# Kernel optimization log

Measured on AMD Instinct MI355X. Metric: run time of the kernel, lower is better.

## Reference

```python
import jax, jax.numpy as jnp
import numpy as np

N_USER, N_ITEM, D, N_LAYER, NNZ, B = 50000, 100000, 64, 3, 2400000, 4096
NEG_SLOPE = 0.2
EPS = 1e-12


def setup_inputs() -> dict:
    key = jax.random.key(0)
    ks = jax.random.split(key, 12)
    N = N_USER + N_ITEM
    user_emb = jax.random.normal(ks[0], (N_USER, D), dtype=jnp.float32) * 0.1
    item_emb = jax.random.normal(ks[1], (N_ITEM, D), dtype=jnp.float32) * 0.1
    rows = jax.random.randint(ks[2], (NNZ,), 0, N, dtype=jnp.int32)
    cols = jax.random.randint(ks[3], (NNZ,), 0, N, dtype=jnp.int32)
    edge_index = jnp.stack([rows, cols])  # [2, nnz] COO indices of sparse L
    # normalized-Laplacian-like positive values, ~1/deg scale
    edge_vals = jax.random.uniform(ks[4], (NNZ,), dtype=jnp.float32) * (1.0 / 16.0)
    scale = 1.0 / np.sqrt(D)
    W1 = jax.random.normal(ks[5], (N_LAYER, D, D), dtype=jnp.float32) * scale
    W2 = jax.random.normal(ks[6], (N_LAYER, D, D), dtype=jnp.float32) * scale
    b1 = jnp.zeros((N_LAYER, D), dtype=jnp.float32)
    b2 = jnp.zeros((N_LAYER, D), dtype=jnp.float32)
    users = jax.random.randint(ks[7], (B,), 1, N_USER + 1, dtype=jnp.int32)      # 1-indexed
    pos_items = jax.random.randint(ks[8], (B,), 1, N_ITEM + 1, dtype=jnp.int32)  # 1-indexed
    neg_items = jax.random.randint(ks[9], (B,), 1, N_ITEM + 1, dtype=jnp.int32)  # 1-indexed
    return {"user_emb": user_emb, "item_emb": item_emb, "edge_vals": edge_vals,
            "W1": W1, "b1": b1, "W2": W2, "b2": b2,
            "edge_index": edge_index, "users": users,
            "pos_items": pos_items, "neg_items": neg_items}


def _spmm(rows, cols, vals, E, num_nodes):
    # sparse COO L @ E : gather source rows, scale by edge value, scatter-add to dest rows
    return jax.ops.segment_sum(vals[:, None] * E[cols], rows, num_segments=num_nodes)


def reference(user_emb, item_emb, edge_vals, W1, b1, W2, b2,
              edge_index, users, pos_items, neg_items):
    n_user = user_emb.shape[0]
    N = n_user + item_emb.shape[0]
    rows, cols = edge_index[0], edge_index[1]
    E = jnp.concatenate([user_emb, item_emb], axis=0)  # [N, d]
    all_E = [E]
    for i in range(W1.shape[0]):
        LE = _spmm(rows, cols, edge_vals, E, N)          # L @ E
        # (L + I) @ E @ W1 + (L@E * E) @ W2  (dropouts are eval-mode identity)
        h = (LE + E) @ W1[i] + b1[i] + (LE * E) @ W2[i] + b2[i]
        E = jax.nn.leaky_relu(h, NEG_SLOPE)
        nrm = jnp.maximum(jnp.linalg.norm(E, axis=1, keepdims=True), EPS)
        all_E.append(E / nrm)  # L2-normalized copy stored; unnormalized E propagates
    all_E = jnp.concatenate(all_E, axis=1)               # [N, d*(1+L)]
    u_emb = all_E[:n_user][users - 1]
    items = all_E[n_user:]
    return u_emb, items[pos_items - 1], items[neg_items - 1]
```

## Files before the change

kernel.cpp:

```cpp
#include <hip/hip_runtime.h>

#define N_USERC 50000
#define N_ITEMC 100000
#define NN      150000
#define DD      64
#define NLAYER  3
#define NNZC    2400000
#define BB      4096
#define NRID    (3*BB)
#define NBKT    147
#define NABLK   586
#define NTILE   4688
#define ELLW    32
#define ELLROWS 150528
#define OVCAP   32768
#define NWPB    97
#define NPREPB  (NWPB + NABLK)
#define NIB     9375
#define NOSB    3072
#define NISB    (NIB + NOSB)

typedef unsigned short ushort_t;
typedef __attribute__((ext_vector_type(8))) short bf16x8;
typedef __attribute__((ext_vector_type(4))) float f32x4;

static __device__ __forceinline__ float bf2f(ushort_t b) {
    unsigned int u = ((unsigned int)b) << 16;
    return __uint_as_float(u);
}
static __device__ __forceinline__ ushort_t f2bf(float f) {
    unsigned int u = __float_as_uint(f);
    u = u + 0x7FFFu + ((u >> 16) & 1u);
    return (ushort_t)(u >> 16);
}

__global__ __launch_bounds__(256) void k_sniffzb(const unsigned int* __restrict__ ue_words,
                                                 int* __restrict__ flag,
                                                 int* __restrict__ bucket_cnt,
                                                 int* __restrict__ ovcnt) {
    int t = threadIdx.x;
    if (t < 64) {
        int cnt = 0;
        for (int i = 0; i < 4; i++) {
            unsigned int w = ue_words[t * 4 + i];
            unsigned int lo = w & 0xFFFFu;
            unsigned int ex = (lo >> 7) & 0xFF;
            if (ex >= 100 && ex <= 132) cnt++;
        }
        for (int m = 1; m < 64; m <<= 1) cnt += __shfl_xor(cnt, m, 64);
        if (t == 0) *flag = (cnt >= 128) ? 1 : 0;
    } else if (t - 64 < NBKT) {
        bucket_cnt[t - 64] = 0;
    } else if (t == 255) {
        *ovcnt = 0;
    }
}

__global__ __launch_bounds__(256) void k_prep(const void* __restrict__ W1,
                                              const void* __restrict__ W2,
                                              const void* __restrict__ b1,
                                              const void* __restrict__ b2,
                                              const int* __restrict__ rows,
                                              const int* __restrict__ flag,
                                              ushort_t* __restrict__ Wfrag,
                                              float* __restrict__ bsum,
                                              int* __restrict__ bucket_cnt) {
    __shared__ int h[NBKT];
    if (blockIdx.x < NWPB) {
        int idx = blockIdx.x * 256 + threadIdx.x;
        int isbf = *flag;
        if (idx < NLAYER * 4 * 4 * 64 * 8) {
            int i    = idx & 7;
            int lane = (idx >> 3) & 63;
            int jt   = (idx >> 9) & 3;
            int s    = (idx >> 11) & 3;
            int l    = idx >> 13;
            int kfull = 32 * (s & 1) + 8 * (lane >> 4) + i;
            int col   = jt * 16 + (lane & 15);
            const void* W = (s < 2) ? W1 : W2;
            size_t off = (size_t)l * 4096 + (size_t)kfull * 64 + col;
            float v = isbf ? bf2f(((const ushort_t*)W)[off]) : ((const float*)W)[off];
            Wfrag[idx] = f2bf(v);
        } else {
            int r = idx - NLAYER * 4 * 4 * 64 * 8;
            if (r < NLAYER * 64) {
                float v1 = isbf ? bf2f(((const ushort_t*)b1)[r]) : ((const float*)b1)[r];
                float v2 = isbf ? bf2f(((const ushort_t*)b2)[r]) : ((const float*)b2)[r];
                bsum[r] = v1 + v2;
            }
        }
    } else {
        int t = threadIdx.x;
        if (t < NBKT) h[t] = 0;
        __syncthreads();
        int e0 = (blockIdx.x - NWPB) * 4096;
#pragma unroll
        for (int i = 0; i < 16; i++) {
            int e = e0 + t + i * 256;
            if (e < NNZC) atomicAdd(&h[rows[e] >> 10], 1);
        }
        __syncthreads();
        if (t < NBKT && h[t]) atomicAdd(&bucket_cnt[t], h[t]);
    }
}

__global__ __launch_bounds__(256) void k_bscan(const int* __restrict__ bucket_cnt,
                                               int* __restrict__ gbase,
                                               int* __restrict__ gcursor) {
    __shared__ int s[256];
    int t = threadIdx.x;
    int v = (t < NBKT) ? bucket_cnt[t] : 0;
    s[t] = v; __syncthreads();
    for (int off = 1; off < 256; off <<= 1) {
        int x = (t >= off) ? s[t - off] : 0;
        __syncthreads();
        s[t] += x;
        __syncthreads();
    }
    if (t < NBKT) { int ex = s[t] - v; gbase[t] = ex; gcursor[t] = ex; }
    if (t == 0) { gbase[NBKT] = NNZC; }
}

__global__ __launch_bounds__(256) void k_phaseA(const int* __restrict__ rows,
                                                const int* __restrict__ cols,
                                                const void* __restrict__ vals,
                                                const int* __restrict__ flag,
                                                int* __restrict__ gcursor,
                                                int2* __restrict__ binned) {
    __shared__ int hist[NBKT], base_[NBKT], lcur[NBKT];
    int t = threadIdx.x;
    int e0 = blockIdx.x * 4096;
    if (t < NBKT) { hist[t] = 0; lcur[t] = 0; }
    __syncthreads();
    int myrow[16];
#pragma unroll
    for (int i = 0; i < 16; i++) {
        int e = e0 + t + i * 256;
        int r = -1;
        if (e < NNZC) { r = rows[e]; atomicAdd(&hist[r >> 10], 1); }
        myrow[i] = r;
    }
    __syncthreads();
    if (t < NBKT && hist[t] > 0) base_[t] = atomicAdd(&gcursor[t], hist[t]);
    __syncthreads();
    int isbf = *flag;
#pragma unroll
    for (int i = 0; i < 16; i++) {
        int e = e0 + t + i * 256;
        if (e < NNZC) {
            int r = myrow[i];
            int bkt = r >> 10;
            int off = atomicAdd(&lcur[bkt], 1);
            int pos = base_[bkt] + off;
            int c = cols[e];
            float v = isbf ? bf2f(((const ushort_t*)vals)[e]) : ((const float*)vals)[e];
            binned[pos] = make_int2(((r & 1023) << 18) | c, __float_as_int(v));
        }
    }
}

__global__ __launch_bounds__(256) void k_phaseB(const int* __restrict__ gbase,
                                                const int2* __restrict__ binned,
                                                int2* __restrict__ ell,
                                                int4* __restrict__ ovbuf,
                                                int* __restrict__ ovcnt) {
    __shared__ int rcur[1024];
    int b = blockIdx.x, t = threadIdx.x;
    int s = gbase[b], e = gbase[b + 1];
    for (int i = t; i < 1024; i += 256) rcur[i] = 0;
    __syncthreads();
    for (int i = s + t; i < e; i += 256) {
        int2 en = binned[i];
        int rl = en.x >> 18;
        int c  = en.x & 0x3FFFF;
        int off = atomicAdd(&rcur[rl], 1);
        if (off < ELLW) {
            ell[((size_t)(b * 1024 + rl)) * ELLW + off] = make_int2(c, en.y);
        } else {
            int p = atomicAdd(ovcnt, 1);
            if (p < OVCAP) ovbuf[p] = make_int4(b * 1024 + rl, c, en.y, 0);
        }
    }
    __syncthreads();
    for (int i = t; i < 1024; i += 256) {
        int start = rcur[i]; if (start > ELLW) start = ELLW;
        int2* rp = ell + ((size_t)(b * 1024 + i)) * ELLW;
        for (int j = start; j < ELLW; j++) rp[j] = make_int2(0, 0);
    }
}

static __device__ __forceinline__ int rid_to_node(int rid,
                                                  const int* users, const int* pos, const int* neg) {
    if (rid < BB)      return users[rid] - 1;
    if (rid < 2 * BB)  return N_USERC + pos[rid - BB] - 1;
    return N_USERC + neg[rid - 2 * BB] - 1;
}

__global__ __launch_bounds__(256) void k_initslice(const void* __restrict__ ue,
                                                   const void* __restrict__ ie,
                                                   const int* __restrict__ flag,
                                                   ushort_t* __restrict__ Eb0,
                                                   const int* __restrict__ users,
                                                   const int* __restrict__ pos,
                                                   const int* __restrict__ neg,
                                                   float* __restrict__ out) {
    if (blockIdx.x < NIB) {
        int i4 = blockIdx.x * 256 + threadIdx.x;
        if (i4 >= NN * DD / 4) return;
        int idx = i4 * 4;
        int row = idx >> 6;
        bool isU = row < N_USERC;
        int si = isU ? idx : idx - N_USERC * DD;
        if (*flag) {
            const uint2* src = (const uint2*)((const ushort_t*)(isU ? ue : ie) + si);
            *(uint2*)(Eb0 + idx) = *src;
        } else {
            const float* src = (const float*)(isU ? ue : ie) + si;
            ushort_t o[4];
#pragma unroll
            for (int k = 0; k < 4; k++) o[k] = f2bf(src[k]);
            *(uint2*)(Eb0 + idx) = *(uint2*)o;
        }
    } else {
        int rid  = (blockIdx.x - NIB) * 4 + (threadIdx.x >> 6);
        int lane = threadIdx.x & 63;
        if (rid >= NRID) return;
        int node = rid_to_node(rid, users, pos, neg);
        bool isU = node < N_USERC;
        int si = (isU ? node : node - N_USERC) * DD + lane;
        float v = (*flag) ? bf2f(isU ? ((const ushort_t*)ue)[si] : ((const ushort_t*)ie)[si])
                          : (isU ? ((const float*)ue)[si] : ((const float*)ie)[si]);
        out[(size_t)rid * 256 + lane] = v;
    }
}

__global__ __launch_bounds__(256) void k_layer(const int2* __restrict__ ell,
                                               const int4* __restrict__ ovbuf,
                                               const int* __restrict__ ovcnt,
                                               const ushort_t* __restrict__ Eb_in,
                                               ushort_t* __restrict__ Eb_out,
                                               const ushort_t* __restrict__ Wfrag,
                                               const float* __restrict__ bsum,
                                               int layer) {
    __shared__ float sLE[32][68];
    __shared__ float sE [32][68];

    int t    = threadIdx.x;
    int wv   = t >> 6;
    int lane = t & 63;
    int oct  = lane >> 3;
    int d8   = (lane & 7) * 8;
    int hl   = lane >> 4;
    int l16  = lane & 15;
    int r0   = blockIdx.x << 5;

    int lr_ = t >> 3;
    int dm_ = (t & 7) * 8;
    uint4 ev = make_uint4(0u, 0u, 0u, 0u);
    {
        int gr = r0 + lr_;
        if (gr < NN) ev = *(const uint4*)(Eb_in + (size_t)gr * DD + dm_);
    }

    int baseRow = r0 + wv * 8;
    int2 pv_c[4], pv_n[4];
    uint4 q_c[4];
#pragma unroll
    for (int v = 0; v < 4; v++)
        pv_c[v] = ell[(size_t)baseRow * ELLW + v * 8 + oct];
#pragma unroll
    for (int v = 0; v < 4; v++)
        q_c[v] = *(const uint4*)(Eb_in + ((size_t)(unsigned)pv_c[v].x << 6) + d8);
#pragma unroll
    for (int v = 0; v < 4; v++)
        pv_n[v] = ell[(size_t)(baseRow + 1) * ELLW + v * 8 + oct];

#pragma unroll
    for (int sub = 0; sub < 8; sub++) {
        uint4 q_n[4];
        int2 pv_n2[4];
        if (sub < 7) {
#pragma unroll
            for (int v = 0; v < 4; v++)
                q_n[v] = *(const uint4*)(Eb_in + ((size_t)(unsigned)pv_n[v].x << 6) + d8);
        }
        if (sub < 6) {
#pragma unroll
            for (int v = 0; v < 4; v++)
                pv_n2[v] = ell[(size_t)(baseRow + sub + 2) * ELLW + v * 8 + oct];
        }
        float acc[8];
#pragma unroll
        for (int k = 0; k < 8; k++) acc[k] = 0.f;
#pragma unroll
        for (int v = 0; v < 4; v++) {
            float w = __int_as_float(pv_c[v].y);
            acc[0] = fmaf(w, __uint_as_float(q_c[v].x << 16),         acc[0]);
            acc[1] = fmaf(w, __uint_as_float(q_c[v].x & 0xffff0000u), acc[1]);
            acc[2] = fmaf(w, __uint_as_float(q_c[v].y << 16),         acc[2]);
            acc[3] = fmaf(w, __uint_as_float(q_c[v].y & 0xffff0000u), acc[3]);
            acc[4] = fmaf(w, __uint_as_float(q_c[v].z << 16),         acc[4]);
            acc[5] = fmaf(w, __uint_as_float(q_c[v].z & 0xffff0000u), acc[5]);
            acc[6] = fmaf(w, __uint_as_float(q_c[v].w << 16),         acc[6]);
            acc[7] = fmaf(w, __uint_as_float(q_c[v].w & 0xffff0000u), acc[7]);
        }
#pragma unroll
        for (int m = 8; m < 64; m <<= 1)
#pragma unroll
            for (int k = 0; k < 8; k++) acc[k] += __shfl_xor(acc[k], m, 64);
        if (oct == 0) {
            int lr = wv * 8 + sub;
            *(float4*)&sLE[lr][d8]     = make_float4(acc[0], acc[1], acc[2], acc[3]);
            *(float4*)&sLE[lr][d8 + 4] = make_float4(acc[4], acc[5], acc[6], acc[7]);
        }
#pragma unroll
        for (int v = 0; v < 4; v++) {
            pv_c[v] = pv_n[v];
            q_c[v]  = q_n[v];
            pv_n[v] = pv_n2[v];
        }
    }

    sE[lr_][dm_ + 0] = __uint_as_float(ev.x << 16);
    sE[lr_][dm_ + 1] = __uint_as_float(ev.x & 0xffff0000u);
    sE[lr_][dm_ + 2] = __uint_as_float(ev.y << 16);
    sE[lr_][dm_ + 3] = __uint_as_float(ev.y & 0xffff0000u);
    sE[lr_][dm_ + 4] = __uint_as_float(ev.z << 16);
    sE[lr_][dm_ + 5] = __uint_as_float(ev.z & 0xffff0000u);
    sE[lr_][dm_ + 6] = __uint_as_float(ev.w << 16);
    sE[lr_][dm_ + 7] = __uint_as_float(ev.w & 0xffff0000u);
    __syncthreads();

    {
        int n = *ovcnt;
        n = (n < OVCAP) ? n : OVCAP;
        if (wv == 0) {
            for (int i = 0; i < n; i++) {
                int4 ov = ovbuf[i];
                if ((unsigned)(ov.x - r0) < 32u) {
                    float w = __int_as_float(ov.z);
                    sLE[ov.x - r0][lane] += w * bf2f(Eb_in[(size_t)ov.y * DD + lane]);
                }
            }
        }
    }
    __syncthreads();

    int rt = wv & 1;
    int j0w = wv >> 1;
    int jtA = 2 * j0w, jtB = 2 * j0w + 1;
    const uint4* wb = (const uint4*)(Wfrag + (size_t)layer * 8192);
    float bsA = bsum[layer * 64 + jtA * 16 + l16];
    float bsB = bsum[layer * 64 + jtB * 16 + l16];

    f32x4 accA = (f32x4){0.f, 0.f, 0.f, 0.f};
    f32x4 accB = (f32x4){0.f, 0.f, 0.f, 0.f};
    int lrow = rt * 16 + l16;

#pragma unroll
    for (int sh = 0; sh < 2; sh++) {
        bf16x8 w1a, w1b, w2a, w2b;
        {
            uint4 qa = wb[(sh * 4 + jtA) * 64 + lane];
            uint4 qb = wb[(sh * 4 + jtB) * 64 + lane];
            uint4 qc = wb[((2 + sh) * 4 + jtA) * 64 + lane];
            uint4 qd = wb[((2 + sh) * 4 + jtB) * 64 + lane];
            __builtin_memcpy(&w1a, &qa, 16);
            __builtin_memcpy(&w1b, &qb, 16);
            __builtin_memcpy(&w2a, &qc, 16);
            __builtin_memcpy(&w2b, &qd, 16);
        }
        const float* pl = &sLE[lrow][sh * 32 + hl * 8];
        const float* pe = &sE [lrow][sh * 32 + hl * 8];
        float4 l0 = *(const float4*)pl, l1 = *(const float4*)(pl + 4);
        float4 e0 = *(const float4*)pe, e1 = *(const float4*)(pe + 4);
        float le[8] = {l0.x, l0.y, l0.z, l0.w, l1.x, l1.y, l1.z, l1.w};
        float ee[8] = {e0.x, e0.y, e0.z, e0.w, e1.x, e1.y, e1.z, e1.w};
        unsigned int u1h[4], u1l[4], u2h[4], u2l[4];
#pragma unroll
        for (int d = 0; d < 4; d++) {
            float s0 = le[2*d]   + ee[2*d];
            float s1 = le[2*d+1] + ee[2*d+1];
            float m0 = le[2*d]   * ee[2*d];
            float m1 = le[2*d+1] * ee[2*d+1];
            asm("v_cvt_pk_bf16_f32 %0, %1, %2" : "=v"(u1h[d]) : "v"(s0), "v"(s1));
            asm("v_cvt_pk_bf16_f32 %0, %1, %2" : "=v"(u2h[d]) : "v"(m0), "v"(m1));
            float s0r = s0 - __uint_as_float(u1h[d] << 16);
            float s1r = s1 - __uint_as_float(u1h[d] & 0xffff0000u);
            float m0r = m0 - __uint_as_float(u2h[d] << 16);
            float m1r = m1 - __uint_as_float(u2h[d] & 0xffff0000u);
            asm("v_cvt_pk_bf16_f32 %0, %1, %2" : "=v"(u1l[d]) : "v"(s0r), "v"(s1r));
            asm("v_cvt_pk_bf16_f32 %0, %1, %2" : "=v"(u2l[d]) : "v"(m0r), "v"(m1r));
        }
        bf16x8 p1h, p1l, p2h, p2l;
        __builtin_memcpy(&p1h, u1h, 16);
        __builtin_memcpy(&p1l, u1l, 16);
        __builtin_memcpy(&p2h, u2h, 16);
        __builtin_memcpy(&p2l, u2l, 16);

        accA = __builtin_amdgcn_mfma_f32_16x16x32_bf16(p1h, w1a, accA, 0, 0, 0);
        accA = __builtin_amdgcn_mfma_f32_16x16x32_bf16(p1l, w1a, accA, 0, 0, 0);
        accA = __builtin_amdgcn_mfma_f32_16x16x32_bf16(p2h, w2a, accA, 0, 0, 0);
        accA = __builtin_amdgcn_mfma_f32_16x16x32_bf16(p2l, w2a, accA, 0, 0, 0);
        accB = __builtin_amdgcn_mfma_f32_16x16x32_bf16(p1h, w1b, accB, 0, 0, 0);
        accB = __builtin_amdgcn_mfma_f32_16x16x32_bf16(p1l, w1b, accB, 0, 0, 0);
        accB = __builtin_amdgcn_mfma_f32_16x16x32_bf16(p2h, w2b, accB, 0, 0, 0);
        accB = __builtin_amdgcn_mfma_f32_16x16x32_bf16(p2l, w2b, accB, 0, 0, 0);
    }

#pragma unroll
    for (int g = 0; g < 4; g++) {
        int r = r0 + rt * 16 + hl * 4 + g;
        if (r < NN) {
            float hA = accA[g] + bsA; hA = (hA >= 0.f) ? hA : 0.2f * hA;
            float hB = accB[g] + bsB; hB = (hB >= 0.f) ? hB : 0.2f * hB;
            Eb_out[(size_t)r * DD + jtA * 16 + l16] = f2bf(hA);
            Eb_out[(size_t)r * DD + jtB * 16 + l16] = f2bf(hB);
        }
    }
}

__global__ __launch_bounds__(256) void k_outnorm(const ushort_t* __restrict__ Eb,
                                                 const int* __restrict__ users,
                                                 const int* __restrict__ pos,
                                                 const int* __restrict__ neg,
                                                 float* __restrict__ out,
                                                 int cbase) {
    int rid  = blockIdx.x * 4 + (threadIdx.x >> 6);
    int lane = threadIdx.x & 63;
    if (rid >= NRID) return;
    int node = rid_to_node(rid, users, pos, neg);
    float v = bf2f(Eb[(size_t)node * DD + lane]);
    float p2 = v * v;
    for (int m = 1; m < 64; m <<= 1) p2 += __shfl_xor(p2, m, 64);
    float nr = fmaxf(sqrtf(p2), 1e-12f);
    out[(size_t)rid * 256 + cbase + lane] = v / nr;
}

extern "C" void kernel_launch(void* const* d_in, const int* in_sizes, int n_in,
                              void* d_out, int out_size, void* d_ws, size_t ws_size,
                              hipStream_t stream) {
    const void* ue   = d_in[0];
    const void* ie   = d_in[1];
    const void* ev   = d_in[2];
    const void* W1   = d_in[3];
    const void* b1   = d_in[4];
    const void* W2   = d_in[5];
    const void* b2   = d_in[6];
    const int*  ei   = (const int*)d_in[7];
    const int*  usr  = (const int*)d_in[8];
    const int*  posi = (const int*)d_in[9];
    const int*  negi = (const int*)d_in[10];
    float*      out  = (float*)d_out;

    const int* rows = ei;
    const int* cols = ei + NNZC;

    char* w = (char*)d_ws;
    ushort_t* Eb1     = (ushort_t*)w; w += (size_t)NN * DD * 2;
    int2*   binned    = (int2*)w;   w += (size_t)NNZC * 8;
    ushort_t* Eb0     = (ushort_t*)binned;
    int2*   ell       = (int2*)w;   w += (size_t)ELLROWS * ELLW * 8;
    int4*   ovbuf     = (int4*)w;   w += (size_t)OVCAP * 16;
    int*    ovcnt     = (int*)w;    w += 256;
    int*    gbase     = (int*)w;    w += 1024;
    int*    gcursor   = (int*)w;    w += 1024;
    int*    bucket_cnt= (int*)w;    w += 1024;
    int*    flag      = (int*)w;    w += 256;
    ushort_t* Wfrag   = (ushort_t*)w; w += 49152;
    float*  bsum      = (float*)w;  w += 768;

    k_sniffzb<<<1, 256, 0, stream>>>((const unsigned int*)ue, flag, bucket_cnt, ovcnt);
    k_prep<<<NPREPB, 256, 0, stream>>>(W1, W2, b1, b2, rows, flag, Wfrag, bsum, bucket_cnt);
    k_bscan<<<1, 256, 0, stream>>>(bucket_cnt, gbase, gcursor);
    k_phaseA<<<NABLK, 256, 0, stream>>>(rows, cols, ev, flag, gcursor, binned);
    k_phaseB<<<NBKT, 256, 0, stream>>>(gbase, binned, ell, ovbuf, ovcnt);
    k_initslice<<<NISB, 256, 0, stream>>>(ue, ie, flag, Eb0, usr, posi, negi, out);

    for (int l = 0; l < NLAYER; l++) {
        const ushort_t* ebi = (l & 1) ? Eb1 : Eb0;
        ushort_t*       ebo = (l & 1) ? Eb0 : Eb1;
        k_layer<<<NTILE, 256, 0, stream>>>(ell, ovbuf, ovcnt, ebi, ebo, Wfrag, bsum, l);
        k_outnorm<<<3072, 256, 0, stream>>>(ebo, usr, posi, negi, out, 64 * (l + 1));
    }
}
```

Baseline: 417.9 us.

## Fuse graph-build kernels into one cooperative launch and fold output norm into layers

Replaces the six preprocessing launches with one cooperative kernel that uses grid-wide syncs between the sniff, histogram/weight-prep/init, scan, binning and ELL fill stages. It also moves each layer's normalized-output slice for the previous layer's result into extra blocks of the next layer kernel, leaving one trailing outnorm launch. Eb0 now gets its own workspace buffer instead of aliasing the binned array, which concurrent stages would otherwise overwrite. The aim is to cut launch gaps and tail effects. The cost is grid-sync overhead, a fixed 768-block grid that loops over virtual blocks, and a fallback path kept in case the cooperative launch fails.

```diff
diff --git a/kernel.cpp b/kernel.cpp
--- a/kernel.cpp
+++ b/kernel.cpp
@@ -1,4 +1,7 @@
 #include <hip/hip_runtime.h>
+#include <hip/hip_cooperative_groups.h>
+
+namespace cg = cooperative_groups;
 
 #define N_USERC 50000
 #define N_ITEMC 100000
@@ -15,10 +18,10 @@
 #define ELLROWS 150528
 #define OVCAP   32768
 #define NWPB    97
-#define NPREPB  (NWPB + NABLK)
 #define NIB     9375
 #define NOSB    3072
-#define NISB    (NIB + NOSB)
+#define NV1     (NWPB + NABLK + NIB + NOSB)
+#define CGRID   768
 
 typedef unsigned short ushort_t;
 typedef __attribute__((ext_vector_type(8))) short bf16x8;
@@ -34,10 +37,9 @@
     return (ushort_t)(u >> 16);
 }
 
-__global__ __launch_bounds__(256) void k_sniffzb(const unsigned int* __restrict__ ue_words,
-                                                 int* __restrict__ flag,
-                                                 int* __restrict__ bucket_cnt,
-                                                 int* __restrict__ ovcnt) {
+
+static __device__ void d_sniff0(const unsigned int* ue_words, int* flag,
+                                int* bucket_cnt, int* ovcnt) {
     int t = threadIdx.x;
     if (t < 64) {
         int cnt = 0;
@@ -56,116 +58,145 @@
     }
 }
 
-__global__ __launch_bounds__(256) void k_prep(const void* __restrict__ W1,
-                                              const void* __restrict__ W2,
-                                              const void* __restrict__ b1,
-                                              const void* __restrict__ b2,
-                                              const int* __restrict__ rows,
-                                              const int* __restrict__ flag,
-                                              ushort_t* __restrict__ Wfrag,
-                                              float* __restrict__ bsum,
-                                              int* __restrict__ bucket_cnt) {
-    __shared__ int h[NBKT];
-    if (blockIdx.x < NWPB) {
-        int idx = blockIdx.x * 256 + threadIdx.x;
-        int isbf = *flag;
-        if (idx < NLAYER * 4 * 4 * 64 * 8) {
-            int i    = idx & 7;
-            int lane = (idx >> 3) & 63;
-            int jt   = (idx >> 9) & 3;
-            int s    = (idx >> 11) & 3;
-            int l    = idx >> 13;
-            int kfull = 32 * (s & 1) + 8 * (lane >> 4) + i;
-            int col   = jt * 16 + (lane & 15);
-            const void* W = (s < 2) ? W1 : W2;
-            size_t off = (size_t)l * 4096 + (size_t)kfull * 64 + col;
-            float v = isbf ? bf2f(((const ushort_t*)W)[off]) : ((const float*)W)[off];
-            Wfrag[idx] = f2bf(v);
+static __device__ void d_wprep(int vb, int isbf,
+                               const void* W1, const void* W2,
+                               const void* b1, const void* b2,
+                               ushort_t* Wfrag, float* bsum) {
+    int idx = vb * 256 + threadIdx.x;
+    if (idx < NLAYER * 4 * 4 * 64 * 8) {
+        int i    = idx & 7;
+        int lane = (idx >> 3) & 63;
+        int jt   = (idx >> 9) & 3;
+        int s    = (idx >> 11) & 3;
+        int l    = idx >> 13;
+        int kfull = 32 * (s & 1) + 8 * (lane >> 4) + i;
+        int col   = jt * 16 + (lane & 15);
+        const void* W = (s < 2) ? W1 : W2;
+        size_t off = (size_t)l * 4096 + (size_t)kfull * 64 + col;
+        float v = isbf ? bf2f(((const ushort_t*)W)[off]) : ((const float*)W)[off];
+        Wfrag[idx] = f2bf(v);
+    } else {
+        int r = idx - NLAYER * 4 * 4 * 64 * 8;
+        if (r < NLAYER * 64) {
+            float v1 = isbf ? bf2f(((const ushort_t*)b1)[r]) : ((const float*)b1)[r];
+            float v2 = isbf ? bf2f(((const ushort_t*)b2)[r]) : ((const float*)b2)[r];
+            bsum[r] = v1 + v2;
+        }
+    }
+}
+
+static __device__ void d_hist(int vb, const int* rows, int* bucket_cnt, int* sh) {
+    int t = threadIdx.x;
+    if (t < NBKT) sh[t] = 0;
+    __syncthreads();
+    int e0 = vb * 4096;
+#pragma unroll
+    for (int i = 0; i < 16; i++) {
+        int e = e0 + t + i * 256;
+        if (e < NNZC) atomicAdd(&sh[rows[e] >> 10], 1);
+    }
+    __syncthreads();
+    if (t < NBKT && sh[t]) atomicAdd(&bucket_cnt[t], sh[t]);
+    __syncthreads();
+}
+
+static __device__ void d_init(int vb, int isbf, const void* ue, const void* ie,
+                              ushort_t* Eb0) {
+    int i4 = vb * 256 + threadIdx.x;
+    if (i4 < NN * DD / 4) {
+        int idx = i4 * 4;
+        int row = idx >> 6;
+        bool isU = row < N_USERC;
+        int si = isU ? idx : idx - N_USERC * DD;
+        if (isbf) {
+            const uint2* src = (const uint2*)((const ushort_t*)(isU ? ue : ie) + si);
+            *(uint2*)(Eb0 + idx) = *src;
         } else {
-            int r = idx - NLAYER * 4 * 4 * 64 * 8;
-            if (r < NLAYER * 64) {
-                float v1 = isbf ? bf2f(((const ushort_t*)b1)[r]) : ((const float*)b1)[r];
-                float v2 = isbf ? bf2f(((const ushort_t*)b2)[r]) : ((const float*)b2)[r];
-                bsum[r] = v1 + v2;
-            }
-        }
-    } else {
-        int t = threadIdx.x;
-        if (t < NBKT) h[t] = 0;
-        __syncthreads();
-        int e0 = (blockIdx.x - NWPB) * 4096;
-#pragma unroll
-        for (int i = 0; i < 16; i++) {
-            int e = e0 + t + i * 256;
-            if (e < NNZC) atomicAdd(&h[rows[e] >> 10], 1);
-        }
-        __syncthreads();
-        if (t < NBKT && h[t]) atomicAdd(&bucket_cnt[t], h[t]);
-    }
-}
-
-__global__ __launch_bounds__(256) void k_bscan(const int* __restrict__ bucket_cnt,
-                                               int* __restrict__ gbase,
-                                               int* __restrict__ gcursor) {
-    __shared__ int s[256];
+            const float* src = (const float*)(isU ? ue : ie) + si;
+            ushort_t o[4];
+#pragma unroll
+            for (int k = 0; k < 4; k++) o[k] = f2bf(src[k]);
+            *(uint2*)(Eb0 + idx) = *(uint2*)o;
+        }
+    }
+}
+
+static __device__ __forceinline__ int rid_to_node(int rid,
+                                                  const int* users, const int* pos, const int* neg) {
+    if (rid < BB)      return users[rid] - 1;
+    if (rid < 2 * BB)  return N_USERC + pos[rid - BB] - 1;
+    return N_USERC + neg[rid - 2 * BB] - 1;
+}
+
+static __device__ void d_slice0(int vb, int isbf, const void* ue, const void* ie,
+                                const int* users, const int* pos, const int* neg,
+                                float* out) {
+    int rid  = vb * 4 + (threadIdx.x >> 6);
+    int lane = threadIdx.x & 63;
+    if (rid < NRID) {
+        int node = rid_to_node(rid, users, pos, neg);
+        bool isU = node < N_USERC;
+        int si = (isU ? node : node - N_USERC) * DD + lane;
+        float v = isbf ? bf2f(isU ? ((const ushort_t*)ue)[si] : ((const ushort_t*)ie)[si])
+                       : (isU ? ((const float*)ue)[si] : ((const float*)ie)[si]);
+        out[(size_t)rid * 256 + lane] = v;
+    }
+}
+
+static __device__ void d_bscan(const int* bucket_cnt, int* gbase, int* gcursor,
+                               int* sh) {
     int t = threadIdx.x;
     int v = (t < NBKT) ? bucket_cnt[t] : 0;
-    s[t] = v; __syncthreads();
+    sh[t] = v; __syncthreads();
     for (int off = 1; off < 256; off <<= 1) {
-        int x = (t >= off) ? s[t - off] : 0;
+        int x = (t >= off) ? sh[t - off] : 0;
         __syncthreads();
-        s[t] += x;
+        sh[t] += x;
         __syncthreads();
     }
-    if (t < NBKT) { int ex = s[t] - v; gbase[t] = ex; gcursor[t] = ex; }
+    if (t < NBKT) { int ex = sh[t] - v; gbase[t] = ex; gcursor[t] = ex; }
     if (t == 0) { gbase[NBKT] = NNZC; }
-}
-
-__global__ __launch_bounds__(256) void k_phaseA(const int* __restrict__ rows,
-                                                const int* __restrict__ cols,
-                                                const void* __restrict__ vals,
-                                                const int* __restrict__ flag,
-                                                int* __restrict__ gcursor,
-                                                int2* __restrict__ binned) {
-    __shared__ int hist[NBKT], base_[NBKT], lcur[NBKT];
+    __syncthreads();
+}
+
+static __device__ void d_phaseA(int vb, int isbf,
+                                const int* rows, const int* cols, const void* vals,
+                                int* gcursor, int2* binned,
+                                int* shh, int* shb, int* shl) {
     int t = threadIdx.x;
-    int e0 = blockIdx.x * 4096;
-    if (t < NBKT) { hist[t] = 0; lcur[t] = 0; }
+    int e0 = vb * 4096;
+    if (t < NBKT) { shh[t] = 0; shl[t] = 0; }
     __syncthreads();
     int myrow[16];
 #pragma unroll
     for (int i = 0; i < 16; i++) {
         int e = e0 + t + i * 256;
         int r = -1;
-        if (e < NNZC) { r = rows[e]; atomicAdd(&hist[r >> 10], 1); }
+        if (e < NNZC) { r = rows[e]; atomicAdd(&shh[r >> 10], 1); }
         myrow[i] = r;
     }
     __syncthreads();
-    if (t < NBKT && hist[t] > 0) base_[t] = atomicAdd(&gcursor[t], hist[t]);
-    __syncthreads();
-    int isbf = *flag;
+    if (t < NBKT && shh[t] > 0) shb[t] = atomicAdd(&gcursor[t], shh[t]);
+    __syncthreads();
 #pragma unroll
     for (int i = 0; i < 16; i++) {
         int e = e0 + t + i * 256;
         if (e < NNZC) {
             int r = myrow[i];
             int bkt = r >> 10;
-            int off = atomicAdd(&lcur[bkt], 1);
-            int pos = base_[bkt] + off;
+            int off = atomicAdd(&shl[bkt], 1);
+            int pos = shb[bkt] + off;
             int c = cols[e];
             float v = isbf ? bf2f(((const ushort_t*)vals)[e]) : ((const float*)vals)[e];
             binned[pos] = make_int2(((r & 1023) << 18) | c, __float_as_int(v));
         }
     }
-}
-
-__global__ __launch_bounds__(256) void k_phaseB(const int* __restrict__ gbase,
-                                                const int2* __restrict__ binned,
-                                                int2* __restrict__ ell,
-                                                int4* __restrict__ ovbuf,
-                                                int* __restrict__ ovcnt) {
-    __shared__ int rcur[1024];
-    int b = blockIdx.x, t = threadIdx.x;
+    __syncthreads();
+}
+
+static __device__ void d_phaseB(int b, const int* gbase, const int2* binned,
+                                int2* ell, int4* ovbuf, int* ovcnt, int* rcur) {
+    int t = threadIdx.x;
     int s = gbase[b], e = gbase[b + 1];
     for (int i = t; i < 1024; i += 256) rcur[i] = 0;
     __syncthreads();
@@ -187,51 +218,99 @@
         int2* rp = ell + ((size_t)(b * 1024 + i)) * ELLW;
         for (int j = start; j < ELLW; j++) rp[j] = make_int2(0, 0);
     }
-}
-
-static __device__ __forceinline__ int rid_to_node(int rid,
-                                                  const int* users, const int* pos, const int* neg) {
-    if (rid < BB)      return users[rid] - 1;
-    if (rid < 2 * BB)  return N_USERC + pos[rid - BB] - 1;
-    return N_USERC + neg[rid - 2 * BB] - 1;
-}
-
-__global__ __launch_bounds__(256) void k_initslice(const void* __restrict__ ue,
-                                                   const void* __restrict__ ie,
-                                                   const int* __restrict__ flag,
-                                                   ushort_t* __restrict__ Eb0,
-                                                   const int* __restrict__ users,
-                                                   const int* __restrict__ pos,
-                                                   const int* __restrict__ neg,
-                                                   float* __restrict__ out) {
-    if (blockIdx.x < NIB) {
-        int i4 = blockIdx.x * 256 + threadIdx.x;
-        if (i4 >= NN * DD / 4) return;
-        int idx = i4 * 4;
-        int row = idx >> 6;
-        bool isU = row < N_USERC;
-        int si = isU ? idx : idx - N_USERC * DD;
-        if (*flag) {
-            const uint2* src = (const uint2*)((const ushort_t*)(isU ? ue : ie) + si);
-            *(uint2*)(Eb0 + idx) = *src;
+    __syncthreads();
+}
+
+__global__ __launch_bounds__(256) void k_build(const unsigned int* ue_words,
+                                               const void* ue, const void* ie,
+                                               const void* W1, const void* W2,
+                                               const void* b1, const void* b2,
+                                               const int* rows, const int* cols,
+                                               const void* vals,
+                                               const int* users, const int* pos,
+                                               const int* neg,
+                                               int* flag, int* bucket_cnt,
+                                               int* ovcnt, int* gbase, int* gcursor,
+                                               ushort_t* Wfrag, float* bsum,
+                                               int2* binned, int2* ell,
+                                               int4* ovbuf, ushort_t* Eb0,
+                                               float* out) {
+    __shared__ int shA[1024];
+    __shared__ int shB[NBKT], shC[NBKT], shD[NBKT];
+    cg::grid_group g = cg::this_grid();
+
+    if (blockIdx.x == 0) d_sniff0(ue_words, flag, bucket_cnt, ovcnt);
+    g.sync();
+    int isbf = *flag;
+
+    for (int vb = blockIdx.x; vb < NV1; vb += CGRID) {
+        if (vb < NWPB) {
+            d_wprep(vb, isbf, W1, W2, b1, b2, Wfrag, bsum);
+        } else if (vb < NWPB + NABLK) {
+            d_hist(vb - NWPB, rows, bucket_cnt, shA);
+        } else if (vb < NWPB + NABLK + NIB) {
+            d_init(vb - NWPB - NABLK, isbf, ue, ie, Eb0);
         } else {
-            const float* src = (const float*)(isU ? ue : ie) + si;
-            ushort_t o[4];
-#pragma unroll
-            for (int k = 0; k < 4; k++) o[k] = f2bf(src[k]);
-            *(uint2*)(Eb0 + idx) = *(uint2*)o;
-        }
-    } else {
-        int rid  = (blockIdx.x - NIB) * 4 + (threadIdx.x >> 6);
-        int lane = threadIdx.x & 63;
-        if (rid >= NRID) return;
-        int node = rid_to_node(rid, users, pos, neg);
-        bool isU = node < N_USERC;
-        int si = (isU ? node : node - N_USERC) * DD + lane;
-        float v = (*flag) ? bf2f(isU ? ((const ushort_t*)ue)[si] : ((const ushort_t*)ie)[si])
-                          : (isU ? ((const float*)ue)[si] : ((const float*)ie)[si]);
-        out[(size_t)rid * 256 + lane] = v;
-    }
+            d_slice0(vb - NWPB - NABLK - NIB, isbf, ue, ie, users, pos, neg, out);
+        }
+    }
+    g.sync();
+
+    if (blockIdx.x == 0) d_bscan(bucket_cnt, gbase, gcursor, shA);
+    g.sync();
+
+    for (int vb = blockIdx.x; vb < NABLK; vb += CGRID)
+        d_phaseA(vb, isbf, rows, cols, vals, gcursor, binned, shB, shC, shD);
+    g.sync();
+
+    for (int vb = blockIdx.x; vb < NBKT; vb += CGRID)
+        d_phaseB(vb, gbase, binned, ell, ovbuf, ovcnt, shA);
+}
+
+__global__ __launch_bounds__(256) void k_sniffzb(const unsigned int* __restrict__ ue_words,
+                                                 int* __restrict__ flag,
+                                                 int* __restrict__ bucket_cnt,
+                                                 int* __restrict__ ovcnt) {
+    d_sniff0(ue_words, flag, bucket_cnt, ovcnt);
+}
+
+__global__ __launch_bounds__(256) void k_prep(const void* W1, const void* W2,
+                                              const void* b1, const void* b2,
+                                              const int* rows, const int* flag,
+                                              ushort_t* Wfrag, float* bsum,
+                                              int* bucket_cnt) {
+    __shared__ int sh[NBKT];
+    int isbf = *flag;
+    if (blockIdx.x < NWPB) d_wprep(blockIdx.x, isbf, W1, W2, b1, b2, Wfrag, bsum);
+    else                   d_hist(blockIdx.x - NWPB, rows, bucket_cnt, sh);
+}
+
+__global__ __launch_bounds__(256) void k_bscan(const int* bucket_cnt,
+                                               int* gbase, int* gcursor) {
+    __shared__ int sh[256];
+    d_bscan(bucket_cnt, gbase, gcursor, sh);
+}
+
+__global__ __launch_bounds__(256) void k_phaseA(const int* rows, const int* cols,
+                                                const void* vals, const int* flag,
+                                                int* gcursor, int2* binned) {
+    __shared__ int shh[NBKT], shb[NBKT], shl[NBKT];
+    d_phaseA(blockIdx.x, *flag, rows, cols, vals, gcursor, binned, shh, shb, shl);
+}
+
+__global__ __launch_bounds__(256) void k_phaseB(const int* gbase, const int2* binned,
+                                                int2* ell, int4* ovbuf, int* ovcnt) {
+    __shared__ int rcur[1024];
+    d_phaseB(blockIdx.x, gbase, binned, ell, ovbuf, ovcnt, rcur);
+}
+
+__global__ __launch_bounds__(256) void k_initslice(const void* ue, const void* ie,
+                                                   const int* flag, ushort_t* Eb0,
+                                                   const int* users, const int* pos,
+                                                   const int* neg, float* out) {
+    int isbf = *flag;
+    if (blockIdx.x < NIB) d_init(blockIdx.x, isbf, ue, ie, Eb0);
+    else                  d_slice0(blockIdx.x - NIB, isbf, ue, ie, users, pos, neg, out);
 }
 
 __global__ __launch_bounds__(256) void k_layer(const int2* __restrict__ ell,
@@ -241,13 +320,31 @@
                                                ushort_t* __restrict__ Eb_out,
                                                const ushort_t* __restrict__ Wfrag,
                                                const float* __restrict__ bsum,
+                                               const int* __restrict__ users,
+                                               const int* __restrict__ pos,
+                                               const int* __restrict__ neg,
+                                               float* __restrict__ out,
                                                int layer) {
     __shared__ float sLE[32][68];
     __shared__ float sE [32][68];
 
     int t    = threadIdx.x;
+    int lane = t & 63;
+
+    if (blockIdx.x >= NTILE) {
+        int rid = (blockIdx.x - NTILE) * 4 + (t >> 6);
+        if (rid < NRID) {
+            int node = rid_to_node(rid, users, pos, neg);
+            float v = bf2f(Eb_in[(size_t)node * DD + lane]);
+            float p2 = v * v;
+            for (int m = 1; m < 64; m <<= 1) p2 += __shfl_xor(p2, m, 64);
+            float nr = fmaxf(sqrtf(p2), 1e-12f);
+            out[(size_t)rid * 256 + 64 * layer + lane] = v / nr;
+        }
+        return;
+    }
+
     int wv   = t >> 6;
-    int lane = t & 63;
     int oct  = lane >> 3;
     int d8   = (lane & 7) * 8;
     int hl   = lane >> 4;
@@ -458,8 +555,8 @@
 
     char* w = (char*)d_ws;
     ushort_t* Eb1     = (ushort_t*)w; w += (size_t)NN * DD * 2;
+    ushort_t* Eb0     = (ushort_t*)w; w += (size_t)NN * DD * 2;
     int2*   binned    = (int2*)w;   w += (size_t)NNZC * 8;
-    ushort_t* Eb0     = (ushort_t*)binned;
     int2*   ell       = (int2*)w;   w += (size_t)ELLROWS * ELLW * 8;
     int4*   ovbuf     = (int4*)w;   w += (size_t)OVCAP * 16;
     int*    ovcnt     = (int*)w;    w += 256;
@@ -470,17 +567,39 @@
     ushort_t* Wfrag   = (ushort_t*)w; w += 49152;
     float*  bsum      = (float*)w;  w += 768;
 
-    k_sniffzb<<<1, 256, 0, stream>>>((const unsigned int*)ue, flag, bucket_cnt, ovcnt);
-    k_prep<<<NPREPB, 256, 0, stream>>>(W1, W2, b1, b2, rows, flag, Wfrag, bsum, bucket_cnt);
-    k_bscan<<<1, 256, 0, stream>>>(bucket_cnt, gbase, gcursor);
-    k_phaseA<<<NABLK, 256, 0, stream>>>(rows, cols, ev, flag, gcursor, binned);
-    k_phaseB<<<NBKT, 256, 0, stream>>>(gbase, binned, ell, ovbuf, ovcnt);
-    k_initslice<<<NISB, 256, 0, stream>>>(ue, ie, flag, Eb0, usr, posi, negi, out);
+    const unsigned int* ue_words = (const unsigned int*)ue;
+
+    void* args[] = {
+        (void*)&ue_words, (void*)&ue, (void*)&ie,
+        (void*)&W1, (void*)&W2, (void*)&b1, (void*)&b2,
+        (void*)&rows, (void*)&cols, (void*)&ev,
+        (void*)&usr, (void*)&posi, (void*)&negi,
+        (void*)&flag, (void*)&bucket_cnt, (void*)&ovcnt,
+        (void*)&gbase, (void*)&gcursor,
+        (void*)&Wfrag, (void*)&bsum,
+        (void*)&binned, (void*)&ell, (void*)&ovbuf,
+        (void*)&Eb0, (void*)&out
+    };
+    hipError_t cerr = hipLaunchCooperativeKernel((const void*)k_build,
+                                                 dim3(CGRID), dim3(256),
+                                                 args, 0, stream);
+    if (cerr != hipSuccess) {
+        k_sniffzb<<<1, 256, 0, stream>>>(ue_words, flag, bucket_cnt, ovcnt);
+        k_prep<<<NWPB + NABLK, 256, 0, stream>>>(W1, W2, b1, b2, rows, flag,
+                                                 Wfrag, bsum, bucket_cnt);
+        k_bscan<<<1, 256, 0, stream>>>(bucket_cnt, gbase, gcursor);
+        k_phaseA<<<NABLK, 256, 0, stream>>>(rows, cols, ev, flag, gcursor, binned);
+        k_phaseB<<<NBKT, 256, 0, stream>>>(gbase, binned, ell, ovbuf, ovcnt);
+        k_initslice<<<NIB + NOSB, 256, 0, stream>>>(ue, ie, flag, Eb0,
+                                                    usr, posi, negi, out);
+    }
 
     for (int l = 0; l < NLAYER; l++) {
         const ushort_t* ebi = (l & 1) ? Eb1 : Eb0;
         ushort_t*       ebo = (l & 1) ? Eb0 : Eb1;
-        k_layer<<<NTILE, 256, 0, stream>>>(ell, ovbuf, ovcnt, ebi, ebo, Wfrag, bsum, l);
-        k_outnorm<<<3072, 256, 0, stream>>>(ebo, usr, posi, negi, out, 64 * (l + 1));
-    }
-}
+        int grid = (l == 0) ? NTILE : (NTILE + NOSB);
+        k_layer<<<grid, 256, 0, stream>>>(ell, ovbuf, ovcnt, ebi, ebo, Wfrag, bsum,
+                                          usr, posi, negi, out, l);
+    }
+    k_outnorm<<<3072, 256, 0, stream>>>(Eb1, usr, posi, negi, out, 64 * NLAYER);
+}
```

After: 773.1 us. 85.0% more time.
